# Kernel optimization log

Measured on AMD Instinct MI355X. Metric: run time of the kernel, lower is better.

The kernel has to match this reference:

```python
import jax, jax.numpy as jnp
import numpy as np
import math

C_CURV = 1.0          # manifold curvature c
KH = KW = 3
STRIDE = (1, 1)
PADDING = (1, 1)
DILATION = (1, 1)
IN_CH = 64            # includes time channel
OUT_CH = 64           # excludes time channel


def setup_inputs() -> dict:
    key = jax.random.key(0)
    k1, k2, k3 = jax.random.split(key, 3)
    B, H, W = 32, 64, 64
    x = jax.random.normal(k1, (B, H, W, IN_CH), dtype=jnp.float32)
    kk = KH * KW
    lin_in = (IN_CH - 1) * kk + 1  # 568
    stdv = math.sqrt(2.0 / ((IN_CH - 1) * kk))
    weight = jax.random.uniform(k2, (OUT_CH, lin_in), minval=-stdv, maxval=stdv, dtype=jnp.float32)
    bias = jax.random.uniform(k3, (OUT_CH,), minval=-stdv, maxval=stdv, dtype=jnp.float32)
    return {"x": x, "weight": weight, "bias": bias}


def _im2col(x):
    """x: [B,H,W,C] -> gathered patches [B,h_out,w_out,KH,KW,C] (torch Unfold semantics)."""
    B, H, W, C = x.shape
    xp = jnp.pad(x, ((0, 0), (PADDING[0], PADDING[0]), (PADDING[1], PADDING[1]), (0, 0)))
    h_out = (H + 2 * PADDING[0] - DILATION[0] * (KH - 1) - 1) // STRIDE[0] + 1
    w_out = (W + 2 * PADDING[1] - DILATION[1] * (KW - 1) - 1) // STRIDE[1] + 1
    rows = STRIDE[0] * jnp.arange(h_out)[:, None] + DILATION[0] * jnp.arange(KH)[None, :]  # [h_out,KH]
    cols = STRIDE[1] * jnp.arange(w_out)[:, None] + DILATION[1] * jnp.arange(KW)[None, :]  # [w_out,KW]
    g = xp[:, rows[:, None, :, None], cols[None, :, None, :], :]  # [B,h_out,w_out,KH,KW,C]
    return g, h_out, w_out


def reference(x, weight, bias):
    B = x.shape[0]
    kk = KH * KW
    g, h_out, w_out = _im2col(x)
    L = h_out * w_out
    # Time channel (channel 0) over kernel positions, clamped to sqrt(c)
    t = jnp.maximum(g[..., 0].reshape(B, L, kk), jnp.sqrt(jnp.float32(C_CURV)))
    t_rescaled = jnp.sqrt(jnp.sum(t * t, axis=-1, keepdims=True) - (kk - 1) * C_CURV)
    # Space channels in kernel-major, channel-minor order (matches torch reshape/transpose)
    s = g[..., 1:].reshape(B, L, kk * (IN_CH - 1))
    feat = jnp.concatenate([t_rescaled, s], axis=-1)  # [B, L, 568]
    # LorentzLinear: linear on features, recompute time from space norm
    y_space = jnp.einsum('blf,of->blo', feat, weight) + bias
    y_time = jnp.sqrt(jnp.sum(y_space * y_space, axis=-1, keepdims=True) + C_CURV)
    out = jnp.concatenate([y_time, y_space], axis=-1)
    return out.reshape(B, h_out, w_out, OUT_CH + 1)
```

## Files before the change

kernel.cpp:

```cpp
#include <hip/hip_runtime.h>
#include <cstdint>
#include <cstddef>

typedef __attribute__((ext_vector_type(4))) short short4v;
typedef __attribute__((ext_vector_type(8))) short short8v;
typedef __attribute__((ext_vector_type(4))) float floatx4;

#define LIN 568

__device__ __forceinline__ short f32_to_bf16(float f) {
  unsigned u = __builtin_bit_cast(unsigned, f);
  u += 0x7fffu + ((u >> 16) & 1u);
  return (short)(u >> 16);
}
__device__ __forceinline__ float bf16_to_f32(short s) {
  return __builtin_bit_cast(float, ((unsigned)(unsigned short)s) << 16);
}

__global__ void prep_weight(const float* __restrict__ w, short* __restrict__ wfragg) {
  int i = blockIdx.x * 256 + threadIdx.x;
  if (i >= 9 * 2 * 4 * 64 * 8) return;
  int j    = i & 7;
  int lane = (i >> 3) & 63;
  int nb   = (i >> 9) & 3;
  int half = (i >> 11) & 1;
  int tap  = i >> 12;
  int n = nb * 16 + (lane & 15);
  int c = half * 32 + ((lane >> 4) << 3) + j;
  float v = (c == 0) ? 0.0f : w[n * LIN + 1 + tap * 63 + (c - 1)];
  wfragg[i] = f32_to_bf16(v);
}

__launch_bounds__(256, 2)
__global__ void lconv_main(const float* __restrict__ x, const float* __restrict__ w,
                           const float* __restrict__ bias, const short* __restrict__ wfragg,
                           float* __restrict__ out) {
  __shared__ short xt[6 * 66 * 72];

  const int tid = threadIdx.x;
  const int bb = blockIdx.x >> 4;
  const int h0 = (blockIdx.x & 15) << 2;
  const float* xb = x + (size_t)bb * (64 * 64 * 64);

  const int lane = tid & 63;
  const int l15 = lane & 15;
  const int q = lane >> 4;
  const int wv = tid >> 6;

  const short* wfl = wfragg + lane * 8;
  short8v b0[4], b1[4], b2[4];
#pragma unroll
  for (int nb = 0; nb < 4; ++nb) {
    b0[nb] = *(const short8v*)(wfl + 0 * 2048 + nb * 512);
    b1[nb] = *(const short8v*)(wfl + 1 * 2048 + nb * 512);
    b2[nb] = *(const short8v*)(wfl + 2 * 2048 + nb * 512);
  }
  float bj[4], w0j[4];
#pragma unroll
  for (int nb = 0; nb < 4; ++nb) {
    int n = nb * 16 + l15;
    bj[nb] = bias[n];
    w0j[nb] = w[n * LIN];
  }

#pragma unroll
  for (int i = 0; i < 12; ++i) {
    int idx = i * 256 + tid;
    int row = idx >> 9;
    int rem = idx & 511;
    int col = rem >> 3;
    int ch8 = (rem & 7) << 3;
    int h = h0 - 1 + row;
    float4 v0 = {0.f, 0.f, 0.f, 0.f}, v1 = {0.f, 0.f, 0.f, 0.f};
    if ((unsigned)h < 64u) {
      const float* p = xb + ((h * 64 + col) * 64 + ch8);
      v0 = *(const float4*)p;
      v1 = *(const float4*)(p + 4);
    }
    short8v o;
    o[0] = f32_to_bf16(v0.x); o[1] = f32_to_bf16(v0.y);
    o[2] = f32_to_bf16(v0.z); o[3] = f32_to_bf16(v0.w);
    o[4] = f32_to_bf16(v1.x); o[5] = f32_to_bf16(v1.y);
    o[6] = f32_to_bf16(v1.z); o[7] = f32_to_bf16(v1.w);
    *(short8v*)&xt[(row * 66 + col + 1) * 72 + ch8] = o;
  }
  if (tid < 96) {
    int r = tid >> 4;
    int cc = (tid >> 3) & 1;
    int ch8 = (tid & 7) << 3;
    short8v z = {0, 0, 0, 0, 0, 0, 0, 0};
    *(short8v*)&xt[(r * 66 + cc * 65) * 72 + ch8] = z;
  }
  __syncthreads();

  floatx4 acc[4][4];
#pragma unroll
  for (int mb = 0; mb < 4; ++mb)
#pragma unroll
    for (int nb = 0; nb < 4; ++nb) acc[mb][nb] = floatx4{0.f, 0.f, 0.f, 0.f};

#pragma unroll
  for (int step = 0; step < 18; ++step) {
    const int tap = step >> 1, half = step & 1;
    const int kh = tap / 3, kw = tap % 3;

    short8v bn[4];
    if (step + 3 < 18) {
#pragma unroll
      for (int nb = 0; nb < 4; ++nb)
        bn[nb] = *(const short8v*)(wfl + (step + 3) * 2048 + nb * 512);
    }

    const short* ab = &xt[((wv + kh) * 66 + kw + l15) * 72 + half * 32 + q * 8];
    short8v a[4];
#pragma unroll
    for (int mb = 0; mb < 4; ++mb)
      a[mb] = *(const short8v*)(ab + mb * 16 * 72);

#pragma unroll
    for (int mb = 0; mb < 4; ++mb) {
#pragma unroll
      for (int nb = 0; nb < 4; ++nb)
        acc[mb][nb] = __builtin_amdgcn_mfma_f32_16x16x32_bf16(a[mb], b0[nb], acc[mb][nb], 0, 0, 0);
    }
#pragma unroll
    for (int nb = 0; nb < 4; ++nb) { b0[nb] = b1[nb]; b1[nb] = b2[nb]; b2[nb] = bn[nb]; }
  }

  float tres_v;
  {
    float ss = 0.f;
#pragma unroll
    for (int dh = 0; dh < 3; ++dh)
#pragma unroll
      for (int dw = 0; dw < 3; ++dw) {
        float tv = bf16_to_f32(xt[((wv + dh) * 66 + lane + dw) * 72]);
        tv = fmaxf(tv, 1.0f);
        ss += tv * tv;
      }
    tres_v = sqrtf(ss - 8.0f);
  }

#pragma unroll
  for (int mb = 0; mb < 4; ++mb) {
#pragma unroll
    for (int r = 0; r < 4; ++r) {
      int pcol = mb * 16 + q * 4 + r;
      float tr = __shfl(tres_v, pcol);
      float v0 = acc[mb][0][r] + bj[0] + tr * w0j[0];
      float v1 = acc[mb][1][r] + bj[1] + tr * w0j[1];
      float v2 = acc[mb][2][r] + bj[2] + tr * w0j[2];
      float v3 = acc[mb][3][r] + bj[3] + tr * w0j[3];
      float ss = v0 * v0 + v1 * v1 + v2 * v2 + v3 * v3;
      ss += __shfl_xor(ss, 1);
      ss += __shfl_xor(ss, 2);
      ss += __shfl_xor(ss, 4);
      ss += __shfl_xor(ss, 8);
      float* ob = out + (size_t)((bb * 64 + h0 + wv) * 64 + pcol) * 65;
      if (l15 == 0) ob[0] = sqrtf(ss + 1.0f);
      ob[1 + l15]  = v0;
      ob[17 + l15] = v1;
      ob[33 + l15] = v2;
      ob[49 + l15] = v3;
    }
  }
}

extern "C" void kernel_launch(void* const* d_in, const int* in_sizes, int n_in,
                              void* d_out, int out_size, void* d_ws, size_t ws_size,
                              hipStream_t stream) {
  const float* x = (const float*)d_in[0];
  const float* w = (const float*)d_in[1];
  const float* b = (const float*)d_in[2];
  float* out = (float*)d_out;
  short* wfragg = (short*)d_ws;

  prep_weight<<<144, 256, 0, stream>>>(w, wfragg);
  lconv_main<<<32 * 16, 256, 0, stream>>>(x, w, b, wfragg, out);
}
```

Before: 99.22 us.

## Split input tile staging to overlap last rows' loads with first-tap MFMAs

The shared-memory tile fill is split in two. Rows 0-3 are loaded before the first barrier, and rows 4-5 are issued after it, so their global loads overlap the first kernel row of MFMA steps (kh=0), which only read rows wv..wv+1. A second barrier before the kh>=1 steps makes sure the later rows are visible. This adds a barrier and extra live registers during the first steps, and the overlap depends on how the compiler schedules the loads relative to the MFMAs.

```diff
diff --git a/kernel.cpp b/kernel.cpp
--- a/kernel.cpp
+++ b/kernel.cpp
@@ -64,7 +64,7 @@
   }
 
 #pragma unroll
-  for (int i = 0; i < 12; ++i) {
+  for (int i = 0; i < 8; ++i) {
     int idx = i * 256 + tid;
     int row = idx >> 9;
     int rem = idx & 511;
@@ -84,7 +84,7 @@
     o[6] = f32_to_bf16(v1.z); o[7] = f32_to_bf16(v1.w);
     *(short8v*)&xt[(row * 66 + col + 1) * 72 + ch8] = o;
   }
-  if (tid < 96) {
+  if (tid < 64) {
     int r = tid >> 4;
     int cc = (tid >> 3) & 1;
     int ch8 = (tid & 7) << 3;
@@ -93,14 +93,42 @@
   }
   __syncthreads();
 
+#pragma unroll
+  for (int i = 8; i < 12; ++i) {
+    int idx = i * 256 + tid;
+    int row = idx >> 9;
+    int rem = idx & 511;
+    int col = rem >> 3;
+    int ch8 = (rem & 7) << 3;
+    int h = h0 - 1 + row;
+    float4 v0 = {0.f, 0.f, 0.f, 0.f}, v1 = {0.f, 0.f, 0.f, 0.f};
+    if ((unsigned)h < 64u) {
+      const float* p = xb + ((h * 64 + col) * 64 + ch8);
+      v0 = *(const float4*)p;
+      v1 = *(const float4*)(p + 4);
+    }
+    short8v o;
+    o[0] = f32_to_bf16(v0.x); o[1] = f32_to_bf16(v0.y);
+    o[2] = f32_to_bf16(v0.z); o[3] = f32_to_bf16(v0.w);
+    o[4] = f32_to_bf16(v1.x); o[5] = f32_to_bf16(v1.y);
+    o[6] = f32_to_bf16(v1.z); o[7] = f32_to_bf16(v1.w);
+    *(short8v*)&xt[(row * 66 + col + 1) * 72 + ch8] = o;
+  }
+  if (tid < 32) {
+    int r = 4 + (tid >> 4);
+    int cc = (tid >> 3) & 1;
+    int ch8 = (tid & 7) << 3;
+    short8v z = {0, 0, 0, 0, 0, 0, 0, 0};
+    *(short8v*)&xt[(r * 66 + cc * 65) * 72 + ch8] = z;
+  }
+
   floatx4 acc[4][4];
 #pragma unroll
   for (int mb = 0; mb < 4; ++mb)
 #pragma unroll
     for (int nb = 0; nb < 4; ++nb) acc[mb][nb] = floatx4{0.f, 0.f, 0.f, 0.f};
 
-#pragma unroll
-  for (int step = 0; step < 18; ++step) {
+  auto do_step = [&](int step) {
     const int tap = step >> 1, half = step & 1;
     const int kh = tap / 3, kw = tap % 3;
 
@@ -125,7 +153,15 @@
     }
 #pragma unroll
     for (int nb = 0; nb < 4; ++nb) { b0[nb] = b1[nb]; b1[nb] = b2[nb]; b2[nb] = bn[nb]; }
-  }
+  };
+
+#pragma unroll
+  for (int step = 0; step < 6; ++step) do_step(step);
+
+  __syncthreads();
+
+#pragma unroll
+  for (int step = 6; step < 18; ++step) do_step(step);
 
   float tres_v;
   {
```

Result: no change. 98.24 us (-1.0%).
